# Kernel optimization log

Hardware: AMD Instinct MI355X
Metric: run time of the kernel (lower is better)

## Reference

```python
import jax, jax.numpy as jnp
import numpy as np
from jax import lax

REPR_IN = (32, 16, 8)   # multiplicities of l=0,1,2 fields
SIZE = 5                # cubic kernel size (odd)
PAD = SIZE // 2


def setup_inputs() -> dict:
    key = jax.random.key(0)
    k1, k2 = jax.random.split(key)
    c_in = sum(mul * (2 * l + 1) for l, mul in enumerate(REPR_IN))   # 120
    n_non_scalar = sum(REPR_IN[1:])                                   # 24
    x = jax.random.normal(k1, (2, c_in, 48, 48, 48), dtype=jnp.float32)
    # SE3Convolution materialized as its effective dense conv kernel [O, I, D, H, W]
    fan_in = c_in * SIZE ** 3
    w_gate = jax.random.normal(k2, (n_non_scalar, c_in, SIZE, SIZE, SIZE), dtype=jnp.float32) / np.sqrt(fan_in)
    return {"x": x, "w_gate": w_gate}


def reference(x, w_gate):
    B, _, X, Y, Z = x.shape
    # Gate branch: 3D conv (same padding) -> sigmoid, one scalar gate per non-scalar field
    g = jax.nn.sigmoid(
        lax.conv_general_dilated(
            x, w_gate,
            window_strides=(1, 1, 1),
            padding=[(PAD, PAD)] * 3,
            dimension_numbers=("NCDHW", "OIDHW", "NCDHW"),
        )
    )  # [B, n_non_scalar, X, Y, Z]

    parts = []
    begin_x = 0
    begin_g = 0
    for l, mul in enumerate(REPR_IN):
        if mul == 0:
            continue
        dim = 2 * l + 1
        field_x = x[:, begin_x:begin_x + mul * dim]
        if l == 0:
            # scalar activation on the l=0 block
            parts.append(jax.nn.relu(field_x))
        else:
            # broadcast gate over the 2l+1 components of each field copy
            fx = field_x.reshape(B, mul, dim, X, Y, Z)
            fg = g[:, begin_g:begin_g + mul][:, :, None]      # [B, mul, 1, X, Y, Z]
            begin_g += mul
            parts.append((fx * fg).reshape(B, mul * dim, X, Y, Z))
        begin_x += mul * dim
    return jnp.concatenate(parts, axis=1)
```

## Files before the change

kernel.cpp:

```cpp
#include <hip/hip_runtime.h>

typedef __attribute__((ext_vector_type(8))) short short8;
typedef __attribute__((ext_vector_type(4))) float f32x4;

#define SDIM 48
#define SS   (48*48)
#define SSS  (48*48*48)
#define CIN  120
#define CIP  128
#define NCO  24
#define ZP   52
#define NTAP 125

#define WP_USHORTS (4*25*5*32*32)
#define WP_BYTES   ((size_t)WP_USHORTS*2)
#define XT_USHORTS ((size_t)2*48*48*ZP*CIP)
#define XT_BYTES   (XT_USHORTS*2)
#define WTOT_F32   (NCO*CIN*NTAP)

#define A_CHUNKS 1664
#define GLP      25

__device__ __forceinline__ unsigned short f2bf(float f){
    unsigned u = __float_as_uint(f);
    u = (u + 0x7FFFu + ((u >> 16) & 1u)) >> 16;
    return (unsigned short)u;
}

__device__ __forceinline__ void gload_lds16(const unsigned short* g, unsigned short* l)
{
    __builtin_amdgcn_global_load_lds(
        (const __attribute__((address_space(1))) unsigned int*)g,
        (__attribute__((address_space(3))) unsigned int*)l,
        16, 0, 0);
}


__global__ __launch_bounds__(256)
void transpose_x(const float* __restrict__ x, unsigned short* __restrict__ xt)
{
    __shared__ unsigned short sm[CIN*50];
    int bid = blockIdx.x;
    const int iy = bid % 48; bid /= 48;
    const int ix = bid % 48;
    const int b  = bid / 48;
    const int tid = threadIdx.x;

    const float* __restrict__ src = x + (size_t)b*CIN*SSS + ((size_t)ix*48 + iy)*48;
    for (int idx = tid; idx < CIN*48; idx += 256) {
        int ci = idx / 48, z = idx - ci*48;
        sm[ci*50 + z] = f2bf(src[(size_t)ci*SSS + z]);
    }
    __syncthreads();
    unsigned short* __restrict__ dst = xt + (((size_t)(b*48 + ix)*48) + iy)*ZP*CIP;
    for (int odx = tid; odx < ZP*CIP; odx += 256) {
        int zp = odx >> 7, ci = odx & 127;
        int z = zp - 2;
        unsigned short v = 0;
        if (ci < CIN && (unsigned)z < 48u) v = sm[ci*50 + z];
        dst[odx] = v;
    }
}

__global__ __launch_bounds__(256)
void repack_w_bf16(const float* __restrict__ w, unsigned short* __restrict__ wp)
{
    int idx = blockIdx.x*256 + threadIdx.x;
    if (idx >= WP_USHORTS) return;
    int cik = idx & 31;
    int co  = (idx >> 5) & 31;
    int dz  = (idx >> 10) % 5;
    int t   = (idx / 5120) % 25;
    int cc  = idx / 128000;
    int ci  = cc*32 + cik;
    float v = 0.f;
    if (co < NCO && ci < CIN)
        v = w[(size_t)(co*CIN + ci)*NTAP + t*5 + dz];
    wp[idx] = f2bf(v);
}

#define MFMA16(a,b,c) __builtin_amdgcn_mfma_f32_16x16x32_bf16(a,b,c,0,0,0)

__global__ __launch_bounds__(128, 3)
void conv_mfma(const unsigned short* __restrict__ xt,
               const unsigned short* __restrict__ wp,
               const float* __restrict__ x,
               float* __restrict__ out)
{
    __shared__ __align__(16) unsigned short As[A_CHUNKS*8];

    int bid = (blockIdx.x & 7) * 144 + (blockIdx.x >> 3);
    const int ccrot = bid & 3;
    const int oyq = bid % 12; bid /= 12;
    const int ox = bid % 48;
    const int b  = bid / 48;

    const int tid = threadIdx.x;
    const int wave = tid >> 6, lane = tid & 63;
    const int l15 = lane & 15, l4 = lane >> 4;
    const int iy0 = oyq*4 - 2;

    const int dxlo = (ox < 2) ? (2 - ox) : 0;
    const int dxhi = (ox > 45) ? (49 - ox) : 4;
    const int ndx  = dxhi - dxlo + 1;

    int goff[13];
    bool ok[13];
#pragma unroll
    for (int k = 0; k < 13; ++k) {
        int L = k*128 + tid;
        int iyl = L / 208, r = L - iyl*208;
        int zp = r >> 2, sf = r & 3;
        int sg = sf ^ ((zp >> 1) & 3);
        int iy = iy0 + iyl;
        ok[k]   = (unsigned)iy < 48u;
        goff[k] = (iy*52 + zp)*128 + sg*8;
    }
    const unsigned short* zsrc = xt + (lane & 31)*8;

    f32x4 acc[2][3][2];
#pragma unroll
    for (int oh = 0; oh < 2; ++oh)
#pragma unroll
      for (int zb = 0; zb < 3; ++zb)
#pragma unroll
        for (int nt = 0; nt < 2; ++nt) acc[oh][zb][nt] = (f32x4){0,0,0,0};

#pragma unroll 1
    for (int icc = 0; icc < 4; ++icc) {
      const int cc = (icc + ccrot) & 3;
#pragma unroll 1
      for (int dxi = 0; dxi < ndx; ++dxi) {
        const int dx = dxlo + dxi;
        const int ix = ox + dx - 2;
        const unsigned short* __restrict__ slab =
            xt + (size_t)(b*48 + ix)*(48*52*128) + cc*32;

        __syncthreads();
#pragma unroll
        for (int k = 0; k < 13; ++k) {
            const unsigned short* src = ok[k] ? (slab + goff[k]) : zsrc;
            gload_lds16(src, As + k*1024 + wave*512);
        }
        asm volatile("s_waitcnt vmcnt(0)" ::: "memory");
        __builtin_amdgcn_sched_barrier(0);
        __syncthreads();

        const unsigned short* __restrict__ wdxb =
            wp + (size_t)cc*128000 + (size_t)dx*25600 + l15*32 + l4*8;
        const char* __restrict__ asb = (const char*)As;
#pragma unroll
        for (int dy = 0; dy < 5; ++dy) {
            const unsigned short* __restrict__ wt = wdxb + dy*5120;
#pragma unroll
            for (int dz = 0; dz < 5; ++dz) {
                short8 b0 = *(const short8*)(wt + dz*1024);
                short8 b1 = *(const short8*)(wt + dz*1024 + 512);
#pragma unroll
                for (int oh = 0; oh < 2; ++oh) {
                    const char* __restrict__ ab = asb + (wave*2 + oh + dy)*3328;
#pragma unroll
                    for (int zb = 0; zb < 3; ++zb) {
                        const int zp = l15 + dz + zb*16;
                        const int off = zp*64 + ((l4 ^ ((zp >> 1) & 3)) << 4);
                        short8 a = *(const short8*)(ab + off);
                        acc[oh][zb][0] = MFMA16(a, b0, acc[oh][zb][0]);
                        acc[oh][zb][1] = MFMA16(a, b1, acc[oh][zb][1]);
                    }
                }
            }
        }
      }
    }

    __syncthreads();
    float* gl = (float*)As;

#pragma unroll
    for (int nt = 0; nt < 2; ++nt) {
        const int co = nt*16 + l15;
        if (co < NCO) {
#pragma unroll
            for (int oh = 0; oh < 2; ++oh)
#pragma unroll
              for (int zb = 0; zb < 3; ++zb)
#pragma unroll
                for (int r = 0; r < 4; ++r) {
                    const int z0 = zb*16 + l4*4 + r;
                    gl[((wave*2 + oh)*48 + z0)*GLP + co] =
                        1.f / (1.f + __expf(-acc[oh][zb][nt][r]));
                }
        }
    }
    __syncthreads();

    for (int i = tid; i < 384; i += 128) {
        const int pnt = i % 192;
        const int half = i / 192;
        const int z = pnt % 48, oyl = pnt / 48;
        const int oy2 = oyq*4 + oyl;
        const size_t sp = ((size_t)ox*48 + oy2)*48 + z;
        const float* __restrict__ xsp = x   + (size_t)b*CIN*SSS + sp;
        float*       __restrict__ osp = out + (size_t)b*CIN*SSS + sp;
        const float* __restrict__ gp = gl + pnt*GLP;
        for (int c = half*60; c < half*60 + 60; ++c) {
            float v = xsp[(size_t)c*SSS];
            float o;
            if (c < 32)       o = v > 0.f ? v : 0.f;
            else if (c < 80)  o = v * gp[(c - 32) / 3];
            else              o = v * gp[16 + (c - 80) / 5];
            osp[(size_t)c*SSS] = o;
        }
    }
}


__global__ __launch_bounds__(256)
void repack_w_f32(const float* __restrict__ w, float* __restrict__ wpf)
{
    int idx = blockIdx.x * 256 + threadIdx.x;
    if (idx >= WTOT_F32) return;
    int co = idx % NCO;
    int t  = idx / NCO;
    wpf[idx] = w[co * (CIN * NTAP) + t];
}

__global__ __launch_bounds__(128)
void gated_act_f32(const float* __restrict__ x,
                   const float* __restrict__ wpf,
                   float* __restrict__ out)
{
    const int gid = blockIdx.x * 128 + threadIdx.x;
    const int oz = gid % SDIM;
    int r = gid / SDIM;
    const int oy = r % SDIM; r /= SDIM;
    const int ox = r % SDIM;
    const int b  = r / SDIM;

    const float* __restrict__ xb = x + (size_t)b * CIN * SSS;
    float acc[NCO];
#pragma unroll
    for (int i = 0; i < NCO; ++i) acc[i] = 0.f;

    int izc[5]; bool okz[5];
#pragma unroll
    for (int dz = 0; dz < 5; ++dz) {
        int iz = oz + dz - 2;
        okz[dz] = (unsigned)iz < (unsigned)SDIM;
        izc[dz] = okz[dz] ? iz : 0;
    }
    for (int ci = 0; ci < CIN; ++ci) {
        const float* __restrict__ xc = xb + (size_t)ci * SSS;
        const float* __restrict__ wc = wpf + ci * (NTAP * NCO);
#pragma unroll 1
        for (int dx = 0; dx < 5; ++dx) {
            const int ix = ox + dx - 2;
            const bool okx = (unsigned)ix < (unsigned)SDIM;
            const int ixc = okx ? ix : 0;
#pragma unroll 1
            for (int dy = 0; dy < 5; ++dy) {
                const int iy = oy + dy - 2;
                const bool oky = (unsigned)iy < (unsigned)SDIM;
                const int iyc = oky ? iy : 0;
                const bool okxy = okx && oky;
                const float* __restrict__ xrow = xc + ixc * SS + iyc * SDIM;
                float xv[5];
#pragma unroll
                for (int dz = 0; dz < 5; ++dz) {
                    float v = xrow[izc[dz]];
                    xv[dz] = (okxy && okz[dz]) ? v : 0.f;
                }
                const float* __restrict__ wr = wc + (dx * 25 + dy * 5) * NCO;
#pragma unroll
                for (int dz = 0; dz < 5; ++dz) {
                    const float v = xv[dz];
#pragma unroll
                    for (int co = 0; co < NCO; ++co)
                        acc[co] = fmaf(v, wr[dz * NCO + co], acc[co]);
                }
            }
        }
    }
    float g[NCO];
#pragma unroll
    for (int co = 0; co < NCO; ++co)
        g[co] = 1.f / (1.f + __expf(-acc[co]));

    const size_t sbase = (size_t)b * CIN * SSS + ox * SS + oy * SDIM + oz;
    float* __restrict__ ob = out + sbase;
    const float* __restrict__ xs = x + sbase;
#pragma unroll
    for (int c = 0; c < 32; ++c) {
        float v = xs[(size_t)c * SSS];
        ob[(size_t)c * SSS] = v > 0.f ? v : 0.f;
    }
#pragma unroll
    for (int m = 0; m < 16; ++m) {
        const float gv = g[m];
#pragma unroll
        for (int k = 0; k < 3; ++k) {
            const int c = 32 + m * 3 + k;
            ob[(size_t)c * SSS] = xs[(size_t)c * SSS] * gv;
        }
    }
#pragma unroll
    for (int m = 0; m < 8; ++m) {
        const float gv = g[16 + m];
#pragma unroll
        for (int k = 0; k < 5; ++k) {
            const int c = 80 + m * 5 + k;
            ob[(size_t)c * SSS] = xs[(size_t)c * SSS] * gv;
        }
    }
}

extern "C" void kernel_launch(void* const* d_in, const int* in_sizes, int n_in,
                              void* d_out, int out_size, void* d_ws, size_t ws_size,
                              hipStream_t stream)
{
    const float* x = (const float*)d_in[0];
    const float* w = (const float*)d_in[1];
    float* out = (float*)d_out;

    if (ws_size >= WP_BYTES + XT_BYTES) {
        unsigned short* wp  = (unsigned short*)d_ws;
        unsigned short* xtb = (unsigned short*)((char*)d_ws + WP_BYTES);
        hipLaunchKernelGGL(repack_w_bf16, dim3((WP_USHORTS + 255) / 256), dim3(256),
                           0, stream, w, wp);
        hipLaunchKernelGGL(transpose_x, dim3(2*48*48), dim3(256), 0, stream, x, xtb);
        hipLaunchKernelGGL(conv_mfma, dim3(2*48*12), dim3(128), 0, stream,
                           xtb, wp, x, out);
    } else if (ws_size >= (size_t)WTOT_F32 * 4) {
        float* wpf = (float*)d_ws;
        hipLaunchKernelGGL(repack_w_f32, dim3((WTOT_F32 + 255) / 256), dim3(256),
                           0, stream, w, wpf);
        hipLaunchKernelGGL(gated_act_f32, dim3(2*SSS/128), dim3(128), 0, stream,
                           x, wpf, out);
    }
}
```

Baseline: 388.6 us.

## Double-buffer LDS input slabs to overlap global loads with MFMA compute

Allocates two LDS buffers for the input slab and issues the async global-to-LDS loads for the next (channel chunk, dx) step right after the barrier, before running MFMAs on the current buffer. This hides global load latency that was previously exposed before each compute phase. It doubles LDS usage per block, which may limit occupancy, and removes the per-block channel-chunk start rotation.

```diff
diff --git a/kernel.cpp b/kernel.cpp
--- a/kernel.cpp
+++ b/kernel.cpp
@@ -19,6 +19,7 @@
 #define WTOT_F32   (NCO*CIN*NTAP)
 
 #define A_CHUNKS 1664
+#define ABUF_USH 13312
 #define GLP      25
 
 __device__ __forceinline__ unsigned short f2bf(float f){
@@ -81,16 +82,27 @@
 
 #define MFMA16(a,b,c) __builtin_amdgcn_mfma_f32_16x16x32_bf16(a,b,c,0,0,0)
 
+#define STAGE(cc_, dx_, p_) do {                                               \
+    const int ix_ = ox + (dx_) - 2;                                            \
+    const unsigned short* __restrict__ slab_ =                                 \
+        xt + (size_t)(b*48 + ix_)*(48*52*128) + (cc_)*32;                      \
+    unsigned short* dst_ = As + (p_)*ABUF_USH + wave*512;                      \
+    _Pragma("unroll")                                                          \
+    for (int k_ = 0; k_ < 13; ++k_) {                                          \
+        const unsigned short* src_ = ok[k_] ? (slab_ + goff[k_]) : zsrc;       \
+        gload_lds16(src_, dst_ + k_*1024);                                     \
+    }                                                                          \
+} while (0)
+
 __global__ __launch_bounds__(128, 3)
 void conv_mfma(const unsigned short* __restrict__ xt,
                const unsigned short* __restrict__ wp,
                const float* __restrict__ x,
                float* __restrict__ out)
 {
-    __shared__ __align__(16) unsigned short As[A_CHUNKS*8];
+    __shared__ __align__(16) unsigned short As[2*ABUF_USH];
 
     int bid = (blockIdx.x & 7) * 144 + (blockIdx.x >> 3);
-    const int ccrot = bid & 3;
     const int oyq = bid % 12; bid /= 12;
     const int ox = bid % 48;
     const int b  = bid / 48;
@@ -126,29 +138,29 @@
 #pragma unroll
         for (int nt = 0; nt < 2; ++nt) acc[oh][zb][nt] = (f32x4){0,0,0,0};
 
+    STAGE(0, dxlo, 0);
+    int pcur = 0;
+
 #pragma unroll 1
-    for (int icc = 0; icc < 4; ++icc) {
-      const int cc = (icc + ccrot) & 3;
+    for (int cc = 0; cc < 4; ++cc) {
 #pragma unroll 1
       for (int dxi = 0; dxi < ndx; ++dxi) {
         const int dx = dxlo + dxi;
-        const int ix = ox + dx - 2;
-        const unsigned short* __restrict__ slab =
-            xt + (size_t)(b*48 + ix)*(48*52*128) + cc*32;
-
-        __syncthreads();
-#pragma unroll
-        for (int k = 0; k < 13; ++k) {
-            const unsigned short* src = ok[k] ? (slab + goff[k]) : zsrc;
-            gload_lds16(src, As + k*1024 + wave*512);
-        }
+
         asm volatile("s_waitcnt vmcnt(0)" ::: "memory");
         __builtin_amdgcn_sched_barrier(0);
         __syncthreads();
 
+        {
+            const int more = (dxi + 1 < ndx);
+            const int cc2 = more ? cc : cc + 1;
+            const int dx2 = more ? dx + 1 : dxlo;
+            if (cc2 < 4) STAGE(cc2, dx2, pcur ^ 1);
+        }
+
         const unsigned short* __restrict__ wdxb =
             wp + (size_t)cc*128000 + (size_t)dx*25600 + l15*32 + l4*8;
-        const char* __restrict__ asb = (const char*)As;
+        const char* __restrict__ asb = (const char*)(As + pcur*ABUF_USH);
 #pragma unroll
         for (int dy = 0; dy < 5; ++dy) {
             const unsigned short* __restrict__ wt = wdxb + dy*5120;
@@ -170,6 +182,7 @@
                 }
             }
         }
+        pcur ^= 1;
       }
     }
 
```

Result: slower. 469.1 us (+20.7%).
